# Performance work log

Measured on AMD Instinct MI355X. Metric: run time of the kernel, lower is better.

Reference implementation:

```python
import jax, jax.numpy as jnp
import numpy as np

EPS = 1e-08


def _norm(H, add):
    # Faithful to GTN.norm: transpose, mask/set diagonal, row-normalize by degree, transpose back.
    # The original O(N^3) mm(deg_inv_diag, H) is expressed as an O(N^2) row scaling (same math).
    Ht = H.T
    n = Ht.shape[0]
    eye = jnp.eye(n, dtype=H.dtype)
    Ht = Ht * (1.0 - eye)
    if add:
        Ht = Ht + eye
    deg = jnp.sum(Ht, axis=1)
    deg_inv = jnp.where(deg == 0, 0.0, 1.0 / (deg + EPS))
    return (deg_inv[:, None] * Ht).T


def _gtconv(A, w):
    # A: [E, N, N]; w: [C, E, 1, 1] -> softmax over E, weighted sum of adjacency channels.
    s = jax.nn.softmax(w[:, :, 0, 0], axis=1)  # [C, E]
    return jnp.einsum('ce,eij->cij', s, A)     # [C, N, N]


def setup_inputs() -> dict:
    key = jax.random.key(0)
    k = jax.random.split(key, 6)
    E, N, C, w_in, w_out = 5, 2048, 2, 256, 64
    A = jax.random.uniform(k[0], (E, N, N), dtype=jnp.float32)
    X = jax.random.normal(k[1], (N, w_in), dtype=jnp.float32)
    conv_w_l0_1 = jax.random.normal(k[2], (C, E, 1, 1), dtype=jnp.float32)
    conv_w_l0_2 = jax.random.normal(k[3], (C, E, 1, 1), dtype=jnp.float32)
    conv_w_l1 = jax.random.normal(k[4], (C, E, 1, 1), dtype=jnp.float32)
    gcn_weight = jax.random.normal(k[5], (w_in, w_out), dtype=jnp.float32) * (1.0 / np.sqrt(w_in))
    return {"A": A, "X": X, "conv_w_l0_1": conv_w_l0_1, "conv_w_l0_2": conv_w_l0_2,
            "conv_w_l1": conv_w_l1, "gcn_weight": gcn_weight}


def reference(A, X, conv_w_l0_1, conv_w_l0_2, conv_w_l1, gcn_weight):
    N = A.shape[1]
    # Layer 0 (first=True): two GTConvs, meta-path composition via bmm.
    a = _gtconv(A, conv_w_l0_1)            # [C, N, N]
    b = _gtconv(A, conv_w_l0_2)            # [C, N, N]
    H = jnp.einsum('cij,cjk->cik', a, b)   # [C, N, N]
    # Layer 1 (first=False): normalize per channel, then compose with new conv.
    H = jax.vmap(lambda h: _norm(h, False))(H)
    a1 = _gtconv(A, conv_w_l1)
    H = jnp.einsum('cij,cjk->cik', H, a1)
    # GCN readout per channel: mm(norm_add(H_c).T, X @ W), relu, concat along features.
    Xw = X @ gcn_weight                     # [N, w_out]
    Hn = jax.vmap(lambda h: _norm(h, True))(H)   # [C, N, N]
    Xc = jax.nn.relu(jnp.einsum('cji,jk->cik', Hn, Xw))  # [C, N, w_out]
    X_ = jnp.transpose(Xc, (1, 0, 2)).reshape(N, -1)     # [N, C*w_out]
    return X_
```

## Files before the change

kernel.cpp:

```cpp
#include <hip/hip_runtime.h>
#include <cstdint>
#include <cstddef>

typedef unsigned short u16;
typedef __attribute__((ext_vector_type(8))) short short8;
typedef __attribute__((ext_vector_type(4))) float v4f;

static constexpr size_t NN = (size_t)2048 * 2048;
#define N2 2048

typedef __attribute__((address_space(1))) const unsigned int guint;
typedef __attribute__((address_space(3))) unsigned int luint;

__device__ __forceinline__ float b2f_bits(uint32_t hi) { union { uint32_t u; float f; } v; v.u = hi; return v.f; }
__device__ __forceinline__ float b2f(u16 x) { return b2f_bits((uint32_t)x << 16); }
__device__ __forceinline__ u16 f2b(float f) {
  union { float f; uint32_t u; } v; v.f = f;
  uint32_t r = v.u + 0x7fffu + ((v.u >> 16) & 1u);
  return (u16)(r >> 16);
}
__device__ __forceinline__ uint4 pack8(const float* f) {
  uint4 u;
  u.x = (uint32_t)f2b(f[0]) | ((uint32_t)f2b(f[1]) << 16);
  u.y = (uint32_t)f2b(f[2]) | ((uint32_t)f2b(f[3]) << 16);
  u.z = (uint32_t)f2b(f[4]) | ((uint32_t)f2b(f[5]) << 16);
  u.w = (uint32_t)f2b(f[6]) | ((uint32_t)f2b(f[7]) << 16);
  return u;
}
__device__ __forceinline__ void unp8(uint4 u, float* f) {
  f[0] = b2f_bits(u.x << 16); f[1] = b2f_bits(u.x & 0xffff0000u);
  f[2] = b2f_bits(u.y << 16); f[3] = b2f_bits(u.y & 0xffff0000u);
  f[4] = b2f_bits(u.z << 16); f[5] = b2f_bits(u.z & 0xffff0000u);
  f[6] = b2f_bits(u.w << 16); f[7] = b2f_bits(u.w & 0xffff0000u);
}
__device__ __forceinline__ float sgprf(float x) {
  union { float f; int i; } v; v.f = x;
  v.i = __builtin_amdgcn_readfirstlane(v.i);
  return v.f;
}

__global__ __launch_bounds__(512, 2) void conv_kernel(
    const float* __restrict__ A, const float* __restrict__ w1,
    const float* __restrict__ w2, const float* __restrict__ w3,
    const float* __restrict__ X, const float* __restrict__ W,
    u16* __restrict__ abf, u16* __restrict__ bbt, u16* __restrict__ a1t,
    u16* __restrict__ a1r, u16* __restrict__ Xwt)
{
  __shared__ u16 LT[4][64 * 64];
  const int t = threadIdx.x;
  const int i0 = blockIdx.y * 64, j0 = blockIdx.x * 64;
  const int m = t >> 3;
  const int cg = t & 7;
  const int n0 = cg * 8;

  float sc[3][2][5];
  {
    const float* wsrc[3] = { w1, w2, w3 };
    for (int q = 0; q < 3; ++q)
      for (int c = 0; c < 2; ++c) {
        float v[5], mx = -1e30f, sum = 0.f;
        #pragma unroll
        for (int e = 0; e < 5; ++e) { v[e] = wsrc[q][c * 5 + e]; mx = fmaxf(mx, v[e]); }
        #pragma unroll
        for (int e = 0; e < 5; ++e) { v[e] = expf(v[e] - mx); sum += v[e]; }
        #pragma unroll
        for (int e = 0; e < 5; ++e) sc[q][c][e] = sgprf(v[e] / sum);
      }
  }

  float av[2][8], bv[2][8], cv[2][8];
  #pragma unroll
  for (int c = 0; c < 2; ++c)
    #pragma unroll
    for (int u = 0; u < 8; ++u) { av[c][u] = 0.f; bv[c][u] = 0.f; cv[c][u] = 0.f; }

  #pragma unroll
  for (int e = 0; e < 5; ++e) {
    const float* base = A + (size_t)e * NN + (size_t)(i0 + m) * N2 + (j0 + n0);
    float4 x0 = ((const float4*)base)[0];
    float4 x1 = ((const float4*)base)[1];
    float f[8] = { x0.x, x0.y, x0.z, x0.w, x1.x, x1.y, x1.z, x1.w };
    #pragma unroll
    for (int c = 0; c < 2; ++c)
      #pragma unroll
      for (int u = 0; u < 8; ++u) {
        av[c][u] += sc[0][c][e] * f[u];
        bv[c][u] += sc[1][c][e] * f[u];
        cv[c][u] += sc[2][c][e] * f[u];
      }
  }

  #pragma unroll
  for (int c = 0; c < 2; ++c) {
    *(uint4*)(abf + (size_t)c * NN + (size_t)(i0 + m) * N2 + (j0 + n0)) = pack8(av[c]);
    *(uint4*)(a1r + (size_t)c * NN + (size_t)(i0 + m) * N2 + (j0 + n0)) = pack8(cv[c]);
  }
  const int swb = ((m >> 3) ^ cg) & 7;
  const int mlo = m & 7;
  #pragma unroll
  for (int c = 0; c < 2; ++c)
    #pragma unroll
    for (int u = 0; u < 8; ++u) {
      const int idx = (n0 + u) * 64 + swb * 8 + mlo;
      LT[c][idx]     = f2b(bv[c][u]);
      LT[2 + c][idx] = f2b(cv[c][u]);
    }
  __syncthreads();
  {
    const int on = t >> 3;
    const int mb = t & 7;
    const int src = on * 64 + (((mb ^ (on >> 3)) & 7) * 8);
    #pragma unroll
    for (int c = 0; c < 2; ++c) {
      *(uint4*)(bbt + (size_t)c * NN + (size_t)(j0 + on) * N2 + (i0 + mb * 8)) =
          *(const uint4*)&LT[c][src];
      *(uint4*)(a1t + (size_t)c * NN + (size_t)(j0 + on) * N2 + (i0 + mb * 8)) =
          *(const uint4*)&LT[2 + c][src];
    }
  }
  if (blockIdx.y < 8) {
    const int n = (int)(blockIdx.y * 32 + blockIdx.x) * 8 + (t >> 6);
    const int k = t & 63;
    float acc = 0.f;
    for (int mm = 0; mm < 256; ++mm)
      acc += X[n * 256 + mm] * W[mm * 64 + k];
    Xwt[(size_t)k * N2 + n] = f2b(acc);
  }
}

template<bool TOUT>
__global__ __launch_bounds__(256, 3) void gemm_kernel(
    const u16* __restrict__ Ain, const u16* __restrict__ Btin,
    u16* __restrict__ Cout, float* __restrict__ csp, float* __restrict__ diag)
{
  const int c = blockIdx.z;
  const u16* Ac = Ain + (size_t)c * NN;
  const u16* Bc = Btin + (size_t)c * NN;
  const int m0 = blockIdx.y * 128, n0 = blockIdx.x * 128;
  const int t = threadIdx.x, w = t >> 6, lane = t & 63;
  const int quad = lane >> 4, r = lane & 15;
  __shared__ u16 SM[128 * 64 + 128 * 64];
  u16* As = SM;
  u16* Bs = SM + 128 * 64;

  v4f zero4 = { 0.f, 0.f, 0.f, 0.f };
  v4f acc[2][8];
  #pragma unroll
  for (int i = 0; i < 2; ++i)
    #pragma unroll
    for (int j = 0; j < 8; ++j) acc[i][j] = zero4;

  const int srow = lane >> 3;
  const int sgran = (lane & 7) ^ srow;

  for (int kt = 0; kt < 2048; kt += 64) {
    __syncthreads();
    #pragma unroll
    for (int i = 0; i < 4; ++i) {
      const int chunk = i * 4 + w;
      const u16* ga = Ac + (size_t)(m0 + chunk * 8 + srow) * N2 + kt + sgran * 8;
      __builtin_amdgcn_global_load_lds((guint*)ga, (luint*)(As + chunk * 512), 16, 0, 0);
    }
    #pragma unroll
    for (int i = 0; i < 4; ++i) {
      const int chunk = i * 4 + w;
      const u16* gb = Bc + (size_t)(n0 + chunk * 8 + srow) * N2 + kt + sgran * 8;
      __builtin_amdgcn_global_load_lds((guint*)gb, (luint*)(Bs + chunk * 512), 16, 0, 0);
    }
    __syncthreads();
    #pragma unroll
    for (int ks = 0; ks < 2; ++ks) {
      const int sl = ((ks * 4 + quad) ^ (r & 7)) * 8;
      short8 af[2], bf[8];
      #pragma unroll
      for (int i = 0; i < 2; ++i)
        af[i] = *(const short8*)(As + (w * 32 + i * 16 + r) * 64 + sl);
      #pragma unroll
      for (int j = 0; j < 8; ++j)
        bf[j] = *(const short8*)(Bs + (j * 16 + r) * 64 + sl);
      #pragma unroll
      for (int i = 0; i < 2; ++i)
        #pragma unroll
        for (int j = 0; j < 8; ++j)
          acc[i][j] = __builtin_amdgcn_mfma_f32_16x16x32_bf16(af[i], bf[j], acc[i][j], 0, 0, 0);
    }
  }
  if (blockIdx.x == blockIdx.y) {
    #pragma unroll
    for (int i = 0; i < 2; ++i) {
      const int rowg = m0 + w * 32 + i * 16 + quad * 4;
      #pragma unroll
      for (int j = 0; j < 8; ++j) {
        const int colg = n0 + j * 16 + r;
        #pragma unroll
        for (int g = 0; g < 4; ++g)
          if (rowg + g == colg) diag[c * N2 + colg] = acc[i][j][g];
      }
    }
  }
  if constexpr (!TOUT) {
    u16* Cc = Cout + (size_t)c * NN;
    #pragma unroll
    for (int i = 0; i < 2; ++i) {
      const int rowg = m0 + w * 32 + i * 16 + quad * 4;
      #pragma unroll
      for (int j = 0; j < 8; ++j) {
        const int colg = n0 + j * 16 + r;
        #pragma unroll
        for (int g = 0; g < 4; ++g)
          Cc[(size_t)(rowg + g) * N2 + colg] = f2b(acc[i][j][g]);
      }
    }
  }
  float s[8];
  #pragma unroll
  for (int j = 0; j < 8; ++j) {
    s[j] = 0.f;
    #pragma unroll
    for (int i = 0; i < 2; ++i)
      #pragma unroll
      for (int g = 0; g < 4; ++g) s[j] += acc[i][j][g];
    s[j] += __shfl_xor(s[j], 16);
    s[j] += __shfl_xor(s[j], 32);
  }
  __syncthreads();
  float* csl = (float*)SM;
  if (quad == 0) {
    #pragma unroll
    for (int j = 0; j < 8; ++j) csl[w * 128 + j * 16 + r] = s[j];
  }
  __syncthreads();
  if (t < 128) {
    const float v = csl[t] + csl[128 + t] + csl[256 + t] + csl[384 + t];
    csp[((size_t)(c * 16) + blockIdx.y) * N2 + n0 + t] = v;
  }
  if constexpr (TOUT) {
    u16* tb = SM;
    u16* Cc = Cout + (size_t)c * NN;
    #pragma unroll
    for (int h = 0; h < 2; ++h) {
      __syncthreads();
      #pragma unroll
      for (int i = 0; i < 2; ++i) {
        #pragma unroll
        for (int jl = 0; jl < 4; ++jl) {
          const int j = h * 4 + jl;
          #pragma unroll
          for (int g = 0; g < 4; ++g)
            tb[(jl * 16 + r) * 136 + (w * 32 + i * 16 + quad * 4 + g)] = f2b(acc[i][j][g]);
        }
      }
      __syncthreads();
      const int rown = t >> 2, seg = t & 3;
      const u16* ps = tb + rown * 136 + seg * 32;
      uint4* pd = (uint4*)(Cc + (size_t)(n0 + h * 64 + rown) * N2 + m0 + seg * 32);
      pd[0] = ((const uint4*)ps)[0];
      pd[1] = ((const uint4*)ps)[1];
      pd[2] = ((const uint4*)ps)[2];
      pd[3] = ((const uint4*)ps)[3];
    }
  }
}

__global__ __launch_bounds__(256) void zgemm_kernel(
    const u16* __restrict__ Ht, const u16* __restrict__ Xwt, float* __restrict__ Zp,
    const float* __restrict__ csp, const float* __restrict__ diag,
    float* __restrict__ ci, float* __restrict__ wv)
{
  const int c = blockIdx.z, split = blockIdx.y;
  const int m0 = blockIdx.x * 128;
  const u16* Ac = Ht + (size_t)c * NN;
  const int t = threadIdx.x, w = t >> 6, lane = t & 63;
  const int quad = lane >> 4, r = lane & 15;
  __shared__ u16 As[128 * 64];
  __shared__ u16 Bs[64 * 64];

  v4f zero4 = { 0.f, 0.f, 0.f, 0.f };
  v4f acc[2][4];
  #pragma unroll
  for (int i = 0; i < 2; ++i)
    #pragma unroll
    for (int j = 0; j < 4; ++j) acc[i][j] = zero4;

  const int srow = lane >> 3;
  const int sgran = (lane & 7) ^ srow;

  for (int kk = 0; kk < 4; ++kk) {
    const int kt = split * 256 + kk * 64;
    __syncthreads();
    #pragma unroll
    for (int i = 0; i < 4; ++i) {
      const int chunk = i * 4 + w;
      const u16* ga = Ac + (size_t)(m0 + chunk * 8 + srow) * N2 + kt + sgran * 8;
      __builtin_amdgcn_global_load_lds((guint*)ga, (luint*)(As + chunk * 512), 16, 0, 0);
    }
    #pragma unroll
    for (int i = 0; i < 2; ++i) {
      const int chunk = i * 4 + w;
      const u16* gb = Xwt + (size_t)(chunk * 8 + srow) * N2 + kt + sgran * 8;
      __builtin_amdgcn_global_load_lds((guint*)gb, (luint*)(Bs + chunk * 512), 16, 0, 0);
    }
    __syncthreads();
    #pragma unroll
    for (int ks = 0; ks < 2; ++ks) {
      const int sl = ((ks * 4 + quad) ^ (r & 7)) * 8;
      short8 af[2], bf[4];
      #pragma unroll
      for (int i = 0; i < 2; ++i)
        af[i] = *(const short8*)(As + (w * 32 + i * 16 + r) * 64 + sl);
      #pragma unroll
      for (int j = 0; j < 4; ++j)
        bf[j] = *(const short8*)(Bs + (j * 16 + r) * 64 + sl);
      #pragma unroll
      for (int i = 0; i < 2; ++i)
        #pragma unroll
        for (int j = 0; j < 4; ++j)
          acc[i][j] = __builtin_amdgcn_mfma_f32_16x16x32_bf16(af[i], bf[j], acc[i][j], 0, 0, 0);
    }
  }
  const size_t pbase = (size_t)(split * 2 + c) * 64;
  #pragma unroll
  for (int i = 0; i < 2; ++i) {
    const int rowg = m0 + w * 32 + i * 16 + quad * 4;
    #pragma unroll
    for (int j = 0; j < 4; ++j) {
      const int colg = j * 16 + r;
      *(v4f*)(Zp + (pbase + colg) * (size_t)N2 + rowg) = acc[i][j];
    }
  }
  if (blockIdx.x == 0 && blockIdx.y == 0) {
    for (int q = t; q < 2048; q += 256) {
      float cs = 0.f;
      #pragma unroll
      for (int s = 0; s < 16; ++s) cs += csp[((size_t)(c * 16) + s) * N2 + q];
      const float deg = cs - diag[c * N2 + q];
      const float v = (deg == 0.f) ? 0.f : 1.f / (deg + 1e-8f);
      ci[c * N2 + q] = v;
      wv[c * N2 + q] = v * deg;
    }
  }
}

__global__ __launch_bounds__(256) void dcol_kernel(
    const u16* __restrict__ Ht, const u16* __restrict__ a1r,
    const float* __restrict__ ci, const float* __restrict__ wv,
    float* __restrict__ dp, float* __restrict__ cp)
{
  const int qg = blockIdx.x, c = blockIdx.y;
  const int p0 = threadIdx.x * 8;
  float dacc[8] = {0,0,0,0,0,0,0,0};
  float cacc[8] = {0,0,0,0,0,0,0,0};
  const u16* hb = Ht  + (size_t)c * NN + (size_t)(qg * 16) * N2 + p0;
  const u16* ab = a1r + (size_t)c * NN + (size_t)(qg * 16) * N2 + p0;
  for (int qq = 0; qq < 16; ++qq) {
    const int q = qg * 16 + qq;
    const float cq = ci[c * N2 + q];
    const float wq = wv[c * N2 + q];
    uint4 hu = *(const uint4*)(hb + (size_t)qq * N2);
    uint4 au = *(const uint4*)(ab + (size_t)qq * N2);
    float h[8], a[8];
    unp8(hu, h); unp8(au, a);
    #pragma unroll
    for (int u = 0; u < 8; ++u) {
      cacc[u] += wq * a[u];
      const float tv = cq * h[u] * a[u];
      dacc[u] += (p0 + u == q) ? 0.f : tv;
    }
  }
  float* dd = dp + (size_t)(c * 128 + qg) * N2 + p0;
  float* cd = cp + (size_t)(c * 128 + qg) * N2 + p0;
  v4f d0 = { dacc[0], dacc[1], dacc[2], dacc[3] };
  v4f d1 = { dacc[4], dacc[5], dacc[6], dacc[7] };
  v4f c0 = { cacc[0], cacc[1], cacc[2], cacc[3] };
  v4f c1 = { cacc[4], cacc[5], cacc[6], cacc[7] };
  *(v4f*)dd = d0; *(v4f*)(dd + 4) = d1;
  *(v4f*)cd = c0; *(v4f*)(cd + 4) = c1;
}

__global__ __launch_bounds__(256) void yfix_kernel(
    const float* __restrict__ Zp, const float* __restrict__ ci,
    const float* __restrict__ diag1, const u16* __restrict__ Xwt,
    u16* __restrict__ Yt)
{
  const int idx = blockIdx.x * 256 + threadIdx.x;
  const int i = idx & 2047, k = (idx >> 11) & 63, c = idx >> 17;
  float z = 0.f;
  #pragma unroll
  for (int s = 0; s < 8; ++s)
    z += Zp[(size_t)((s * 2 + c) * 64 + k) * N2 + i];
  const float xw = b2f(Xwt[(size_t)k * N2 + i]);
  const float y = ci[c * N2 + i] * (z - diag1[c * N2 + i] * xw);
  Yt[(size_t)c * 64 * N2 + (size_t)k * N2 + i] = f2b(y);
}

__global__ void fin_kernel(const float* __restrict__ dp, const float* __restrict__ cp,
                           float* __restrict__ diag2, float* __restrict__ dinv2)
{
  const int idx = blockIdx.x * 256 + threadIdx.x;
  const int c = idx >> 11, i = idx & 2047;
  float ds = 0.f, cs = 0.f;
  for (int b = 0; b < 128; ++b) {
    ds += dp[(size_t)(c * 128 + b) * N2 + i];
    cs += cp[(size_t)(c * 128 + b) * N2 + i];
  }
  const float deg = cs - ds + 1.0f;
  diag2[idx] = ds;
  dinv2[idx] = (deg == 0.f) ? 0.f : 1.f / (deg + 1e-8f);
}

__global__ __launch_bounds__(256) void tgemm_kernel(
    const u16* __restrict__ a1t, const u16* __restrict__ Yt, float* __restrict__ Tp)
{
  const int c = blockIdx.z, split = blockIdx.y;
  const int m0 = blockIdx.x * 128;
  const u16* Ac = a1t + (size_t)c * NN;
  const u16* Bc = Yt + (size_t)c * (64 * (size_t)N2);
  const int t = threadIdx.x, w = t >> 6, lane = t & 63;
  const int quad = lane >> 4, r = lane & 15;
  __shared__ u16 As[128 * 64];
  __shared__ u16 Bs[64 * 64];

  v4f zero4 = { 0.f, 0.f, 0.f, 0.f };
  v4f acc[2][4];
  #pragma unroll
  for (int i = 0; i < 2; ++i)
    #pragma unroll
    for (int j = 0; j < 4; ++j) acc[i][j] = zero4;

  const int srow = lane >> 3;
  const int sgran = (lane & 7) ^ srow;

  for (int kk = 0; kk < 4; ++kk) {
    const int kt = split * 256 + kk * 64;
    __syncthreads();
    #pragma unroll
    for (int i = 0; i < 4; ++i) {
      const int chunk = i * 4 + w;
      const u16* ga = Ac + (size_t)(m0 + chunk * 8 + srow) * N2 + kt + sgran * 8;
      __builtin_amdgcn_global_load_lds((guint*)ga, (luint*)(As + chunk * 512), 16, 0, 0);
    }
    #pragma unroll
    for (int i = 0; i < 2; ++i) {
      const int chunk = i * 4 + w;
      const u16* gb = Bc + (size_t)(chunk * 8 + srow) * N2 + kt + sgran * 8;
      __builtin_amdgcn_global_load_lds((guint*)gb, (luint*)(Bs + chunk * 512), 16, 0, 0);
    }
    __syncthreads();
    #pragma unroll
    for (int ks = 0; ks < 2; ++ks) {
      const int sl = ((ks * 4 + quad) ^ (r & 7)) * 8;
      short8 af[2], bf[4];
      #pragma unroll
      for (int i = 0; i < 2; ++i)
        af[i] = *(const short8*)(As + (w * 32 + i * 16 + r) * 64 + sl);
      #pragma unroll
      for (int j = 0; j < 4; ++j)
        bf[j] = *(const short8*)(Bs + (j * 16 + r) * 64 + sl);
      #pragma unroll
      for (int i = 0; i < 2; ++i)
        #pragma unroll
        for (int j = 0; j < 4; ++j)
          acc[i][j] = __builtin_amdgcn_mfma_f32_16x16x32_bf16(af[i], bf[j], acc[i][j], 0, 0, 0);
    }
  }
  const size_t pbase = (size_t)(split * 2 + c) * 2048;
  #pragma unroll
  for (int i = 0; i < 2; ++i) {
    const int rowg = m0 + w * 32 + i * 16 + quad * 4;
    #pragma unroll
    for (int j = 0; j < 4; ++j) {
      const int colg = j * 16 + r;
      #pragma unroll
      for (int g = 0; g < 4; ++g)
        Tp[(pbase + rowg + g) * 64 + colg] = acc[i][j][g];
    }
  }
}

__global__ void epilogue_kernel(const float* __restrict__ Tp, const float* __restrict__ diag2,
                                const float* __restrict__ dinv2, const u16* __restrict__ Xwt,
                                float* __restrict__ out)
{
  const int idx = blockIdx.x * 256 + threadIdx.x;
  const int k = idx & 63;
  const int c = (idx >> 6) & 1;
  const int i = idx >> 7;
  float T = 0.f;
  #pragma unroll
  for (int s = 0; s < 8; ++s)
    T += Tp[((size_t)(s * 2 + c) * 2048 + i) * 64 + k];
  const float hd = diag2[c * N2 + i];
  const float dv = dinv2[c * N2 + i];
  const float xw = b2f(Xwt[(size_t)k * N2 + i]);
  float v = dv * (T - hd * xw + xw);
  v = v > 0.f ? v : 0.f;
  out[(size_t)i * 128 + c * 64 + k] = v;
}

extern "C" void kernel_launch(void* const* d_in, const int* in_sizes, int n_in,
                              void* d_out, int out_size, void* d_ws, size_t ws_size,
                              hipStream_t stream) {
  const float* A  = (const float*)d_in[0];
  const float* X  = (const float*)d_in[1];
  const float* w1 = (const float*)d_in[2];
  const float* w2 = (const float*)d_in[3];
  const float* w3 = (const float*)d_in[4];
  const float* W  = (const float*)d_in[5];
  float* out = (float*)d_out;
  char* ws = (char*)d_ws;

  u16*   abf   = (u16*)(ws + 0);
  u16*   bbt   = (u16*)(ws + 16777216);
  u16*   a1t   = (u16*)(ws + 33554432);
  u16*   a1r   = (u16*)(ws + 50331648);
  u16*   Ht    = (u16*)(ws + 67108864);
  u16*   Xwt   = (u16*)(ws + 83886080);
  float* cspa  = (float*)(ws + 84148224);
  float* diag1 = (float*)(ws + 84410368);
  float* ci1   = (float*)(ws + 84426752);
  float* w2v   = (float*)(ws + 84443136);
  float* diag2 = (float*)(ws + 84459520);
  float* dinv2 = (float*)(ws + 84475904);
  float* Zp    = (float*)(ws + 0);
  float* dp    = (float*)(ws + 16777216);
  float* cp    = (float*)(ws + 18874368);
  u16*   Yt    = (u16*)(ws + 20971520);
  float* Tp    = (float*)(ws + 50331648);

  conv_kernel<<<dim3(32, 32), 512, 0, stream>>>(A, w1, w2, w3, X, W, abf, bbt, a1t, a1r, Xwt);
  gemm_kernel<true><<<dim3(16, 16, 2), 256, 0, stream>>>(abf, bbt, Ht, cspa, diag1);
  zgemm_kernel<<<dim3(16, 8, 2), 256, 0, stream>>>(Ht, Xwt, Zp, cspa, diag1, ci1, w2v);
  dcol_kernel<<<dim3(128, 2), 256, 0, stream>>>(Ht, a1r, ci1, w2v, dp, cp);
  yfix_kernel<<<1024, 256, 0, stream>>>(Zp, ci1, diag1, Xwt, Yt);
  fin_kernel<<<16, 256, 0, stream>>>(dp, cp, diag2, dinv2);
  tgemm_kernel<<<dim3(16, 8, 2), 256, 0, stream>>>(a1t, Yt, Tp);
  epilogue_kernel<<<1024, 256, 0, stream>>>(Tp, diag2, dinv2, Xwt, out);
}
```

Before: 246.4 us.

## Fuse dcol/yfix/fin/epilogue into GEMM kernels via last-block atomic counters

Merges the degree-column pass, the Y fix-up, the final degree reduction and the epilogue into the zgemm and tgemm kernels. Each step runs in whichever block arrives last on an atomic counter, and the counters are reset by conv_kernel. This cuts the launch count from eight to four and removes separate passes over intermediates. It also halves the transpose LDS buffer in conv_kernel and drops unused template code. In exchange, the tail work is serialized onto single blocks, and correctness now depends on threadfence/atomic ordering.

After: 258.6 us. 4.9% more time.

```diff
diff --git a/kernel.cpp b/kernel.cpp
--- a/kernel.cpp
+++ b/kernel.cpp
@@ -27,12 +27,6 @@
   u.w = (uint32_t)f2b(f[6]) | ((uint32_t)f2b(f[7]) << 16);
   return u;
 }
-__device__ __forceinline__ void unp8(uint4 u, float* f) {
-  f[0] = b2f_bits(u.x << 16); f[1] = b2f_bits(u.x & 0xffff0000u);
-  f[2] = b2f_bits(u.y << 16); f[3] = b2f_bits(u.y & 0xffff0000u);
-  f[4] = b2f_bits(u.z << 16); f[5] = b2f_bits(u.z & 0xffff0000u);
-  f[6] = b2f_bits(u.w << 16); f[7] = b2f_bits(u.w & 0xffff0000u);
-}
 __device__ __forceinline__ float sgprf(float x) {
   union { float f; int i; } v; v.f = x;
   v.i = __builtin_amdgcn_readfirstlane(v.i);
@@ -44,14 +38,16 @@
     const float* __restrict__ w2, const float* __restrict__ w3,
     const float* __restrict__ X, const float* __restrict__ W,
     u16* __restrict__ abf, u16* __restrict__ bbt, u16* __restrict__ a1t,
-    u16* __restrict__ a1r, u16* __restrict__ Xwt)
+    u16* __restrict__ a1r, u16* __restrict__ Xwt, int* __restrict__ counters)
 {
-  __shared__ u16 LT[4][64 * 64];
+  __shared__ u16 LT[2][64 * 64];
   const int t = threadIdx.x;
   const int i0 = blockIdx.y * 64, j0 = blockIdx.x * 64;
   const int m = t >> 3;
   const int cg = t & 7;
   const int n0 = cg * 8;
+
+  if (blockIdx.x == 0 && blockIdx.y == 0 && t < 66) counters[t] = 0;
 
   float sc[3][2][5];
   {
@@ -97,26 +93,23 @@
   }
   const int swb = ((m >> 3) ^ cg) & 7;
   const int mlo = m & 7;
-  #pragma unroll
-  for (int c = 0; c < 2; ++c)
+  const int on = t >> 3;
+  const int mb = t & 7;
+  const int src = on * 64 + (((mb ^ (on >> 3)) & 7) * 8);
+  #pragma unroll
+  for (int c = 0; c < 2; ++c) {
+    if (c == 1) __syncthreads();
     #pragma unroll
     for (int u = 0; u < 8; ++u) {
       const int idx = (n0 + u) * 64 + swb * 8 + mlo;
-      LT[c][idx]     = f2b(bv[c][u]);
-      LT[2 + c][idx] = f2b(cv[c][u]);
-    }
-  __syncthreads();
-  {
-    const int on = t >> 3;
-    const int mb = t & 7;
-    const int src = on * 64 + (((mb ^ (on >> 3)) & 7) * 8);
-    #pragma unroll
-    for (int c = 0; c < 2; ++c) {
-      *(uint4*)(bbt + (size_t)c * NN + (size_t)(j0 + on) * N2 + (i0 + mb * 8)) =
-          *(const uint4*)&LT[c][src];
-      *(uint4*)(a1t + (size_t)c * NN + (size_t)(j0 + on) * N2 + (i0 + mb * 8)) =
-          *(const uint4*)&LT[2 + c][src];
-    }
+      LT[0][idx] = f2b(bv[c][u]);
+      LT[1][idx] = f2b(cv[c][u]);
+    }
+    __syncthreads();
+    *(uint4*)(bbt + (size_t)c * NN + (size_t)(j0 + on) * N2 + (i0 + mb * 8)) =
+        *(const uint4*)&LT[0][src];
+    *(uint4*)(a1t + (size_t)c * NN + (size_t)(j0 + on) * N2 + (i0 + mb * 8)) =
+        *(const uint4*)&LT[1][src];
   }
   if (blockIdx.y < 8) {
     const int n = (int)(blockIdx.y * 32 + blockIdx.x) * 8 + (t >> 6);
@@ -128,7 +121,6 @@
   }
 }
 
-template<bool TOUT>
 __global__ __launch_bounds__(256, 3) void gemm_kernel(
     const u16* __restrict__ Ain, const u16* __restrict__ Btin,
     u16* __restrict__ Cout, float* __restrict__ csp, float* __restrict__ diag)
@@ -198,20 +190,6 @@
       }
     }
   }
-  if constexpr (!TOUT) {
-    u16* Cc = Cout + (size_t)c * NN;
-    #pragma unroll
-    for (int i = 0; i < 2; ++i) {
-      const int rowg = m0 + w * 32 + i * 16 + quad * 4;
-      #pragma unroll
-      for (int j = 0; j < 8; ++j) {
-        const int colg = n0 + j * 16 + r;
-        #pragma unroll
-        for (int g = 0; g < 4; ++g)
-          Cc[(size_t)(rowg + g) * N2 + colg] = f2b(acc[i][j][g]);
-      }
-    }
-  }
   float s[8];
   #pragma unroll
   for (int j = 0; j < 8; ++j) {
@@ -234,7 +212,7 @@
     const float v = csl[t] + csl[128 + t] + csl[256 + t] + csl[384 + t];
     csp[((size_t)(c * 16) + blockIdx.y) * N2 + n0 + t] = v;
   }
-  if constexpr (TOUT) {
+  {
     u16* tb = SM;
     u16* Cc = Cout + (size_t)c * NN;
     #pragma unroll
@@ -263,17 +241,21 @@
 }
 
 __global__ __launch_bounds__(256) void zgemm_kernel(
-    const u16* __restrict__ Ht, const u16* __restrict__ Xwt, float* __restrict__ Zp,
-    const float* __restrict__ csp, const float* __restrict__ diag,
-    float* __restrict__ ci, float* __restrict__ wv)
+    const u16* __restrict__ Ht, const u16* __restrict__ Xwt,
+    const u16* __restrict__ a1r, const float* __restrict__ csp,
+    const float* __restrict__ diag1, float* __restrict__ Zp,
+    float* __restrict__ dp, float* __restrict__ cp,
+    u16* __restrict__ Yt, float* __restrict__ diag2, float* __restrict__ dinv2,
+    int* __restrict__ counters)
 {
-  const int c = blockIdx.z, split = blockIdx.y;
-  const int m0 = blockIdx.x * 128;
+  const int c = blockIdx.z, split = blockIdx.y, mt = blockIdx.x;
+  const int m0 = mt * 128;
   const u16* Ac = Ht + (size_t)c * NN;
   const int t = threadIdx.x, w = t >> 6, lane = t & 63;
   const int quad = lane >> 4, r = lane & 15;
-  __shared__ u16 As[128 * 64];
-  __shared__ u16 Bs[64 * 64];
+  __shared__ u16 SMZ[128 * 64 + 64 * 64];
+  u16* As = SMZ;
+  u16* Bs = SMZ + 128 * 64;
 
   v4f zero4 = { 0.f, 0.f, 0.f, 0.f };
   v4f acc[2][4];
@@ -328,91 +310,118 @@
       *(v4f*)(Zp + (pbase + colg) * (size_t)N2 + rowg) = acc[i][j];
     }
   }
-  if (blockIdx.x == 0 && blockIdx.y == 0) {
+  __syncthreads();
+  float* ci_l = (float*)SMZ;
+  float* wv_l = ci_l + 128;
+  if (t < 128) {
+    const int i = m0 + t;
+    float cs = 0.f;
+    #pragma unroll
+    for (int s = 0; s < 16; ++s) cs += csp[((size_t)(c * 16) + s) * N2 + i];
+    const float deg = cs - diag1[c * N2 + i];
+    const float v = (deg == 0.f) ? 0.f : 1.f / (deg + 1e-8f);
+    ci_l[t] = v;
+    wv_l[t] = v * deg;
+  }
+  __syncthreads();
+  const int j4 = (t & 15) * 4, ig = t >> 4;
+  float dacc[4][4], cacc[4][4];
+  #pragma unroll
+  for (int kk = 0; kk < 4; ++kk) {
+    const int gj = split * 256 + kk * 64 + j4;
+    #pragma unroll
+    for (int u = 0; u < 4; ++u) { dacc[kk][u] = 0.f; cacc[kk][u] = 0.f; }
+    for (int ii = 0; ii < 8; ++ii) {
+      const int i = m0 + ig * 8 + ii;
+      uint2 hu = *(const uint2*)(Ht  + (size_t)c * NN + (size_t)i * N2 + gj);
+      uint2 au = *(const uint2*)(a1r + (size_t)c * NN + (size_t)i * N2 + gj);
+      float h[4], a[4];
+      h[0] = b2f_bits(hu.x << 16); h[1] = b2f_bits(hu.x & 0xffff0000u);
+      h[2] = b2f_bits(hu.y << 16); h[3] = b2f_bits(hu.y & 0xffff0000u);
+      a[0] = b2f_bits(au.x << 16); a[1] = b2f_bits(au.x & 0xffff0000u);
+      a[2] = b2f_bits(au.y << 16); a[3] = b2f_bits(au.y & 0xffff0000u);
+      const float cq = ci_l[ig * 8 + ii];
+      const float wq = wv_l[ig * 8 + ii];
+      #pragma unroll
+      for (int u = 0; u < 4; ++u) {
+        cacc[kk][u] += wq * a[u];
+        const float tv = cq * h[u] * a[u];
+        dacc[kk][u] += (i == gj + u) ? 0.f : tv;
+      }
+    }
+  }
+  float* red = ci_l + 256;
+  __syncthreads();
+  #pragma unroll
+  for (int kk = 0; kk < 4; ++kk)
+    #pragma unroll
+    for (int u = 0; u < 4; ++u) red[ig * 256 + kk * 64 + j4 + u] = dacc[kk][u];
+  __syncthreads();
+  {
+    float v = 0.f;
+    #pragma unroll
+    for (int g = 0; g < 16; ++g) v += red[g * 256 + t];
+    dp[((size_t)(c * 16) + mt) * N2 + split * 256 + t] = v;
+  }
+  __syncthreads();
+  #pragma unroll
+  for (int kk = 0; kk < 4; ++kk)
+    #pragma unroll
+    for (int u = 0; u < 4; ++u) red[ig * 256 + kk * 64 + j4 + u] = cacc[kk][u];
+  __syncthreads();
+  {
+    float v = 0.f;
+    #pragma unroll
+    for (int g = 0; g < 16; ++g) v += red[g * 256 + t];
+    cp[((size_t)(c * 16) + mt) * N2 + split * 256 + t] = v;
+  }
+  __shared__ int yLast, fLast;
+  __syncthreads();
+  if (t == 0) {
+    __threadfence();
+    yLast = (atomicAdd(&counters[mt * 2 + c], 1) == 7);
+    fLast = (atomicAdd(&counters[32 + c], 1) == 127);
+  }
+  __syncthreads();
+  if (yLast) {
+    __threadfence();
+    const int i = m0 + (t & 127), kg = t >> 7;
+    const float civ = ci_l[t & 127];
+    const float d1 = diag1[c * N2 + i];
+    for (int k2 = 0; k2 < 32; ++k2) {
+      const int k = kg * 32 + k2;
+      float z = 0.f;
+      #pragma unroll
+      for (int s = 0; s < 8; ++s)
+        z += Zp[(size_t)((s * 2 + c) * 64 + k) * N2 + i];
+      const float xw = b2f(Xwt[(size_t)k * N2 + i]);
+      Yt[(size_t)(c * 64 + k) * N2 + i] = f2b(civ * (z - d1 * xw));
+    }
+  }
+  if (fLast) {
+    __threadfence();
     for (int q = t; q < 2048; q += 256) {
-      float cs = 0.f;
-      #pragma unroll
-      for (int s = 0; s < 16; ++s) cs += csp[((size_t)(c * 16) + s) * N2 + q];
-      const float deg = cs - diag[c * N2 + q];
-      const float v = (deg == 0.f) ? 0.f : 1.f / (deg + 1e-8f);
-      ci[c * N2 + q] = v;
-      wv[c * N2 + q] = v * deg;
-    }
-  }
-}
-
-__global__ __launch_bounds__(256) void dcol_kernel(
-    const u16* __restrict__ Ht, const u16* __restrict__ a1r,
-    const float* __restrict__ ci, const float* __restrict__ wv,
-    float* __restrict__ dp, float* __restrict__ cp)
+      float ds = 0.f, cs = 0.f;
+      #pragma unroll
+      for (int b = 0; b < 16; ++b) {
+        ds += dp[((size_t)(c * 16) + b) * N2 + q];
+        cs += cp[((size_t)(c * 16) + b) * N2 + q];
+      }
+      const float deg = cs - ds + 1.0f;
+      diag2[c * N2 + q] = ds;
+      dinv2[c * N2 + q] = (deg == 0.f) ? 0.f : 1.f / (deg + 1e-8f);
+    }
+  }
+}
+
+__global__ __launch_bounds__(256) void tgemm_kernel(
+    const u16* __restrict__ a1t, const u16* __restrict__ Yt,
+    float* __restrict__ Tp, const float* __restrict__ diag2,
+    const float* __restrict__ dinv2, const u16* __restrict__ Xwt,
+    float* __restrict__ out, int* __restrict__ counters)
 {
-  const int qg = blockIdx.x, c = blockIdx.y;
-  const int p0 = threadIdx.x * 8;
-  float dacc[8] = {0,0,0,0,0,0,0,0};
-  float cacc[8] = {0,0,0,0,0,0,0,0};
-  const u16* hb = Ht  + (size_t)c * NN + (size_t)(qg * 16) * N2 + p0;
-  const u16* ab = a1r + (size_t)c * NN + (size_t)(qg * 16) * N2 + p0;
-  for (int qq = 0; qq < 16; ++qq) {
-    const int q = qg * 16 + qq;
-    const float cq = ci[c * N2 + q];
-    const float wq = wv[c * N2 + q];
-    uint4 hu = *(const uint4*)(hb + (size_t)qq * N2);
-    uint4 au = *(const uint4*)(ab + (size_t)qq * N2);
-    float h[8], a[8];
-    unp8(hu, h); unp8(au, a);
-    #pragma unroll
-    for (int u = 0; u < 8; ++u) {
-      cacc[u] += wq * a[u];
-      const float tv = cq * h[u] * a[u];
-      dacc[u] += (p0 + u == q) ? 0.f : tv;
-    }
-  }
-  float* dd = dp + (size_t)(c * 128 + qg) * N2 + p0;
-  float* cd = cp + (size_t)(c * 128 + qg) * N2 + p0;
-  v4f d0 = { dacc[0], dacc[1], dacc[2], dacc[3] };
-  v4f d1 = { dacc[4], dacc[5], dacc[6], dacc[7] };
-  v4f c0 = { cacc[0], cacc[1], cacc[2], cacc[3] };
-  v4f c1 = { cacc[4], cacc[5], cacc[6], cacc[7] };
-  *(v4f*)dd = d0; *(v4f*)(dd + 4) = d1;
-  *(v4f*)cd = c0; *(v4f*)(cd + 4) = c1;
-}
-
-__global__ __launch_bounds__(256) void yfix_kernel(
-    const float* __restrict__ Zp, const float* __restrict__ ci,
-    const float* __restrict__ diag1, const u16* __restrict__ Xwt,
-    u16* __restrict__ Yt)
-{
-  const int idx = blockIdx.x * 256 + threadIdx.x;
-  const int i = idx & 2047, k = (idx >> 11) & 63, c = idx >> 17;
-  float z = 0.f;
-  #pragma unroll
-  for (int s = 0; s < 8; ++s)
-    z += Zp[(size_t)((s * 2 + c) * 64 + k) * N2 + i];
-  const float xw = b2f(Xwt[(size_t)k * N2 + i]);
-  const float y = ci[c * N2 + i] * (z - diag1[c * N2 + i] * xw);
-  Yt[(size_t)c * 64 * N2 + (size_t)k * N2 + i] = f2b(y);
-}
-
-__global__ void fin_kernel(const float* __restrict__ dp, const float* __restrict__ cp,
-                           float* __restrict__ diag2, float* __restrict__ dinv2)
-{
-  const int idx = blockIdx.x * 256 + threadIdx.x;
-  const int c = idx >> 11, i = idx & 2047;
-  float ds = 0.f, cs = 0.f;
-  for (int b = 0; b < 128; ++b) {
-    ds += dp[(size_t)(c * 128 + b) * N2 + i];
-    cs += cp[(size_t)(c * 128 + b) * N2 + i];
-  }
-  const float deg = cs - ds + 1.0f;
-  diag2[idx] = ds;
-  dinv2[idx] = (deg == 0.f) ? 0.f : 1.f / (deg + 1e-8f);
-}
-
-__global__ __launch_bounds__(256) void tgemm_kernel(
-    const u16* __restrict__ a1t, const u16* __restrict__ Yt, float* __restrict__ Tp)
-{
-  const int c = blockIdx.z, split = blockIdx.y;
-  const int m0 = blockIdx.x * 128;
+  const int c = blockIdx.z, split = blockIdx.y, mt = blockIdx.x;
+  const int m0 = mt * 128;
   const u16* Ac = a1t + (size_t)c * NN;
   const u16* Bc = Yt + (size_t)c * (64 * (size_t)N2);
   const int t = threadIdx.x, w = t >> 6, lane = t & 63;
@@ -475,26 +484,30 @@
         Tp[(pbase + rowg + g) * 64 + colg] = acc[i][j][g];
     }
   }
-}
-
-__global__ void epilogue_kernel(const float* __restrict__ Tp, const float* __restrict__ diag2,
-                                const float* __restrict__ dinv2, const u16* __restrict__ Xwt,
-                                float* __restrict__ out)
-{
-  const int idx = blockIdx.x * 256 + threadIdx.x;
-  const int k = idx & 63;
-  const int c = (idx >> 6) & 1;
-  const int i = idx >> 7;
-  float T = 0.f;
-  #pragma unroll
-  for (int s = 0; s < 8; ++s)
-    T += Tp[((size_t)(s * 2 + c) * 2048 + i) * 64 + k];
-  const float hd = diag2[c * N2 + i];
-  const float dv = dinv2[c * N2 + i];
-  const float xw = b2f(Xwt[(size_t)k * N2 + i]);
-  float v = dv * (T - hd * xw + xw);
-  v = v > 0.f ? v : 0.f;
-  out[(size_t)i * 128 + c * 64 + k] = v;
+  __shared__ int eLast;
+  __syncthreads();
+  if (t == 0) {
+    __threadfence();
+    eLast = (atomicAdd(&counters[34 + mt * 2 + c], 1) == 7);
+  }
+  __syncthreads();
+  if (eLast) {
+    __threadfence();
+    const int k = t & 63, ig = t >> 6;
+    for (int ii = 0; ii < 32; ++ii) {
+      const int i = m0 + ig * 32 + ii;
+      float T = 0.f;
+      #pragma unroll
+      for (int s = 0; s < 8; ++s)
+        T += Tp[((size_t)(s * 2 + c) * 2048 + i) * 64 + k];
+      const float hd = diag2[c * N2 + i];
+      const float dv = dinv2[c * N2 + i];
+      const float xw = b2f(Xwt[(size_t)k * N2 + i]);
+      float v = dv * (T - hd * xw + xw);
+      v = v > 0.f ? v : 0.f;
+      out[(size_t)i * 128 + c * 64 + k] = v;
+    }
+  }
 }
 
 extern "C" void kernel_launch(void* const* d_in, const int* in_sizes, int n_in,
@@ -517,22 +530,17 @@
   u16*   Xwt   = (u16*)(ws + 83886080);
   float* cspa  = (float*)(ws + 84148224);
   float* diag1 = (float*)(ws + 84410368);
-  float* ci1   = (float*)(ws + 84426752);
-  float* w2v   = (float*)(ws + 84443136);
-  float* diag2 = (float*)(ws + 84459520);
-  float* dinv2 = (float*)(ws + 84475904);
+  float* diag2 = (float*)(ws + 84426752);
+  float* dinv2 = (float*)(ws + 84443136);
+  int*   cnt   = (int*)  (ws + 84459520);
   float* Zp    = (float*)(ws + 0);
   float* dp    = (float*)(ws + 16777216);
-  float* cp    = (float*)(ws + 18874368);
-  u16*   Yt    = (u16*)(ws + 20971520);
+  float* cp    = (float*)(ws + 17039360);
+  u16*   Yt    = (u16*)(ws + 17301504);
   float* Tp    = (float*)(ws + 50331648);
 
-  conv_kernel<<<dim3(32, 32), 512, 0, stream>>>(A, w1, w2, w3, X, W, abf, bbt, a1t, a1r, Xwt);
-  gemm_kernel<true><<<dim3(16, 16, 2), 256, 0, stream>>>(abf, bbt, Ht, cspa, diag1);
-  zgemm_kernel<<<dim3(16, 8, 2), 256, 0, stream>>>(Ht, Xwt, Zp, cspa, diag1, ci1, w2v);
-  dcol_kernel<<<dim3(128, 2), 256, 0, stream>>>(Ht, a1r, ci1, w2v, dp, cp);
-  yfix_kernel<<<1024, 256, 0, stream>>>(Zp, ci1, diag1, Xwt, Yt);
-  fin_kernel<<<16, 256, 0, stream>>>(dp, cp, diag2, dinv2);
-  tgemm_kernel<<<dim3(16, 8, 2), 256, 0, stream>>>(a1t, Yt, Tp);
-  epilogue_kernel<<<1024, 256, 0, stream>>>(Tp, diag2, dinv2, Xwt, out);
-}
+  conv_kernel<<<dim3(32, 32), 512, 0, stream>>>(A, w1, w2, w3, X, W, abf, bbt, a1t, a1r, Xwt, cnt);
+  gemm_kernel<<<dim3(16, 16, 2), 256, 0, stream>>>(abf, bbt, Ht, cspa, diag1);
+  zgemm_kernel<<<dim3(16, 8, 2), 256, 0, stream>>>(Ht, Xwt, a1r, cspa, diag1, Zp, dp, cp, Yt, diag2, dinv2, cnt);
+  tgemm_kernel<<<dim3(16, 8, 2), 256, 0, stream>>>(a1t, Yt, Tp, diag2, dinv2, Xwt, out, cnt);
+}
```
